# Kernel tuning notes

Measured on AMD Instinct MI355X. Metric: run time of the kernel, lower is better.

## Reference

```python
import jax, jax.numpy as jnp
import numpy as np
from jax.scipy.special import erf, digamma, i0

B, L, D, H = 4, 4096, 512, 4
_MAX_SQRT_GRADIENT = 1000.0

@jax.custom_vjp
def sqrt_bound(x):
    return jnp.sqrt(x)

def _sb_fwd(x):
    return jnp.sqrt(x), x

def _sb_bwd(x, g):
    return (g / jnp.sqrt(jnp.clip(4.0 * x, 1.0 / _MAX_SQRT_GRADIENT**2, None)),)

sqrt_bound.defvjp(_sb_fwd, _sb_bwd)

def block_diag_linear(x, w):
    # x: [..., D], w: [h, bw, bw] block-diagonal weight
    h, bw, _ = w.shape
    xr = x.reshape(x.shape[:-1] + (h, bw))
    return jnp.einsum('...hi,hij->...hj', xr, w).reshape(x.shape)

def self_att_pool(x, num_heads):
    n_state = x.shape[-1] // num_heads
    attn = jax.nn.softmax(jnp.einsum('bld,bmd->blm', x, x) / np.float32(np.sqrt(n_state)), axis=-1)
    # max over the sequence axis of the attended values, keepdims -> [B,1,D]
    return jnp.max(jnp.einsum('blm,bmd->bld', attn, x), axis=-2, keepdims=True)

def ripple_transform_hybrid(t, mix_params):
    mix = jax.nn.softmax(mix_params)
    return mix[0] * digamma(t + 1.0) + mix[1] * i0(t)

def ripple_act(data, alpha, beta, mix_params, temperature=1.0):
    def f(d):
        norm = erf(d / (jnp.max(d) * alpha))
        return jnp.sum(ripple_transform_hybrid(norm * beta, mix_params))
    g = jnp.clip(jax.grad(f)(data), -1.0, 1.0)
    return jax.nn.softmax(-g / temperature, axis=-1)  # softmin

def ripplemoe_act(data, weights, alphas, beta, mix_params, temperature=1.0):
    def f(d):
        dmax = jnp.max(d)
        norm = erf(d[None] / (dmax * alphas[:, None, None]))  # [S,B,L]
        t = ripple_transform_hybrid(norm * beta, mix_params)
        w = jax.nn.softmax(weights)
        return jnp.sum(w[:, None, None] * t)
    g = jnp.clip(jax.grad(f)(data), -1.0, 1.0)
    return jax.nn.softmax(-g / temperature, axis=-1)  # softmin

def token_selection(x, cls_w, cls_b, token_weights, prelu_a, ts_weights, ts_alphas, ts_beta, ts_mix):
    scores = jnp.einsum('bld,sd->sbl', x, cls_w) + cls_b[:, None, None]  # [S,B,L]
    p = jnp.where(scores >= 0, scores, prelu_a * scores)  # PReLU
    ts = jax.nn.celu(p) * jax.nn.silu(p) + jax.nn.gelu(p, approximate=False)
    combined = jnp.einsum('s,sbl->bl', jax.nn.selu(token_weights[:, 0]), ts)
    _, idx = jax.lax.top_k(combined, combined.shape[-1])  # k = L, descending permutation
    vals = ts.sum(0)  # [B,L]
    b_idx = jnp.arange(combined.shape[0])[:, None]
    importance = jnp.ones_like(combined).at[b_idx, idx].add(vals)
    return (1.0 + ripplemoe_act(importance, ts_weights, ts_alphas, ts_beta, ts_mix))[..., None]

def _forward(x, attention_space, W_spatial, W_sil, W_ohead, W_out, w_ig, w_ag, a_param,
             cls_w, cls_b, token_weights, prelu_a, ts_weights, ts_alphas, ts_beta, ts_mix,
             pa1_alpha, pa1_beta, pa1_mix, pa2_alpha, pa2_beta, pa2_mix):
    spatial = jnp.einsum('bld,de->ble', x, attention_space) @ W_spatial.T
    # RG-LRU style gating
    gate_x = jax.nn.sigmoid(block_diag_linear(x, w_ig))
    gate_a = jax.nn.sigmoid(block_diag_linear(x, w_ag))
    log_a = -8.0 * jax.nn.softplus(a_param) * gate_a
    normalized_x = x * gate_x * sqrt_bound(1.0 - jnp.exp(2.0 * log_a))
    gated = jnp.exp(log_a) * self_att_pool(spatial, H) + normalized_x
    sparsity = ripple_act(gated @ W_sil.T, pa1_alpha, pa1_beta, pa1_mix)
    attn = (gated * sparsity) @ W_ohead.T
    sel = token_selection(x, cls_w, cls_b, token_weights, prelu_a, ts_weights, ts_alphas, ts_beta, ts_mix)
    out = ripple_act(attn * sel, pa2_alpha, pa2_beta, pa2_mix)
    return out @ W_out.T

def setup_inputs() -> dict:
    key = jax.random.key(0)
    ks = jax.random.split(key, 12)
    lim = float(1.0 / np.sqrt(D))
    xav = float(np.sqrt(6.0 / (2 * D)))
    bw = D // H
    u = jax.random.uniform(ks[8], (D,), jnp.float32, 0.9**2 + 1e-8, 0.999**2 + 1e-8)
    return {
        'x': jax.random.normal(ks[0], (B, L, D), jnp.float32),
        'attention_space': jax.random.uniform(ks[1], (D, D), jnp.float32, -xav, xav),
        'W_spatial': jax.random.uniform(ks[2], (D, D), jnp.float32, -lim, lim),
        'W_sil': jax.random.uniform(ks[3], (D, D), jnp.float32, -lim, lim),
        'W_ohead': jax.random.uniform(ks[4], (D, D), jnp.float32, -lim, lim),
        'W_out': jax.random.uniform(ks[5], (D, D), jnp.float32, -lim, lim),
        'w_ig': jax.random.normal(ks[6], (H, bw, bw), jnp.float32) * np.float32(np.sqrt(1.0 / bw)),
        'w_ag': jax.random.normal(ks[7], (H, bw, bw), jnp.float32) * np.float32(np.sqrt(1.0 / bw)),
        'a_param': jnp.log(jnp.exp(-0.5 * jnp.log(u)) - 1.0),
        'cls_w': jax.random.uniform(ks[9], (H, D), jnp.float32, -lim, lim),
        'cls_b': jax.random.uniform(ks[10], (H,), jnp.float32, -lim, lim),
        'token_weights': jax.random.normal(ks[11], (H, 1), jnp.float32),
        'prelu_a': jnp.array(0.25, jnp.float32),
        'ts_weights': jnp.ones(H, jnp.float32) / H,
        'ts_alphas': jnp.ones(H, jnp.float32),
        'ts_beta': jnp.array(1.0, jnp.float32),
        'ts_mix': jnp.full((2,), 0.5, jnp.float32),
        'pa1_alpha': jnp.array(1.0, jnp.float32),
        'pa1_beta': jnp.array(1.0, jnp.float32),
        'pa1_mix': jnp.full((2,), 0.5, jnp.float32),
        'pa2_alpha': jnp.array(1.0, jnp.float32),
        'pa2_beta': jnp.array(1.0, jnp.float32),
        'pa2_mix': jnp.full((2,), 0.5, jnp.float32),
    }

def reference(x, attention_space, W_spatial, W_sil, W_ohead, W_out, w_ig, w_ag, a_param,
              cls_w, cls_b, token_weights, prelu_a, ts_weights, ts_alphas, ts_beta, ts_mix,
              pa1_alpha, pa1_beta, pa1_mix, pa2_alpha, pa2_beta, pa2_mix):
    return _forward(x, attention_space, W_spatial, W_sil, W_ohead, W_out, w_ig, w_ag, a_param,
                    cls_w, cls_b, token_weights, prelu_a, ts_weights, ts_alphas, ts_beta, ts_mix,
                    pa1_alpha, pa1_beta, pa1_mix, pa2_alpha, pa2_beta, pa2_mix)
```

## Files before the change

kernel.cpp:

```cpp
#include <hip/hip_runtime.h>

typedef unsigned short ushort;
typedef unsigned int uint;
typedef unsigned long long u64;

#define DEV __device__ __forceinline__

typedef __attribute__((ext_vector_type(4))) float f32x4;
typedef __bf16 bf16x8 __attribute__((ext_vector_type(8)));
typedef __attribute__((ext_vector_type(4))) ushort u16x4;
typedef __attribute__((ext_vector_type(8))) ushort u16x8;

static constexpr int B_ = 4, L_ = 4096, D_ = 512;
static constexpr long NE = (long)B_ * L_ * D_;

DEV float b2f(ushort u) { return __uint_as_float(((uint)u) << 16); }
DEV ushort f2b(float f) {
    uint u = __float_as_uint(f);
    uint r = u + 0x7FFFu + ((u >> 16) & 1u);
    return (ushort)(r >> 16);
}
DEV uint mapF(float f) {
    uint b = __float_as_uint(f);
    return (b & 0x80000000u) ? ~b : (b | 0x80000000u);
}
DEV float unmapF(uint u) {
    uint b = (u & 0x80000000u) ? (u & 0x7FFFFFFFu) : ~u;
    return __uint_as_float(b);
}
DEV float rcp_(float x) { return __builtin_amdgcn_rcpf(x); }
DEV float fexp(float x) { return __builtin_amdgcn_exp2f(x * 1.44269504089f); }
DEV float sigm(float x) { return rcp_(1.f + fexp(-x)); }

DEV void gload16(const ushort* g, ushort* l) {
    __builtin_amdgcn_global_load_lds((const __attribute__((address_space(1))) void*)g,
                                     (__attribute__((address_space(3))) void*)l, 16, 0, 0);
}

DEV int xcd_swz(int b, int nwg) {
    int q = nwg >> 3, r = nwg & 7;
    int x = b & 7, i = b >> 3;
    int base = (x < r) ? x * (q + 1) : r * (q + 1) + (x - r) * q;
    return base + i;
}

DEV float trigamma1p(float t) {
    float x = t + 1.f;
    float acc = 0.f;
#pragma unroll
    for (int k = 0; k < 6; k++) { float xx = x + (float)k; acc += rcp_(xx * xx); }
    float y = x + 6.f;
    float iy = rcp_(y), iy2 = iy * iy;
    return acc + iy * (1.f + iy * (0.5f + iy * (0.166666667f + iy2 * (-0.0333333333f + iy2 * 0.0238095238f))));
}
DEV float besselI1(float t) {
    float q = 0.25f * t * t;
    return 0.5f * t * (1.f + q * (0.5f + q * (0.0833333333f + q * (0.00694444444f + q * (3.47222222e-4f + q * 1.15740741e-5f)))));
}
DEV float rippleH(float u, float beta, float mix0, float mix1) {
    float t = beta * erff(u);
    float Tp = mix0 * trigamma1p(t) + mix1 * besselI1(t);
    float ep = 1.12837917f * fexp(-u * u);
    return beta * Tp * ep;
}

DEV void gemm_core(const ushort* __restrict__ A, int lda,
                   const ushort* __restrict__ Bt, int ldb, int K,
                   ushort* __restrict__ Alds, ushort* __restrict__ Blds,
                   f32x4 (&acc)[4][4])
{
    const int tid = threadIdx.x;
    const int lane = tid & 63;
    const int wave = tid >> 6;
    const int wr = wave >> 1, wc = wave & 1;

    const int srow = wave * 16 + (lane >> 2);
    const int skc = (lane & 3) * 8;
    const ushort* Ag0 = A + (size_t)srow * lda + skc;
    const ushort* Ag1 = A + (size_t)(srow + 64) * lda + skc;
    const ushort* Bg0 = Bt + (size_t)srow * ldb + skc;
    const ushort* Bg1 = Bt + (size_t)(srow + 64) * ldb + skc;
    const int wb = wave * 512;

    const int ar = wr * 64 + (lane & 15);
    const int br = wc * 64 + (lane & 15);
    const int kk = (lane >> 4) * 8;

    gload16(Ag0, Alds + wb);
    gload16(Ag1, Alds + 2048 + wb);
    gload16(Bg0, Blds + wb);
    gload16(Bg1, Blds + 2048 + wb);
    __syncthreads();

    int cur = 0;
    for (int k0 = 0; k0 < K; k0 += 32) {
        const int nb = cur ^ 1;
        if (k0 + 32 < K) {
            gload16(Ag0 + k0 + 32, Alds + nb * 4096 + wb);
            gload16(Ag1 + k0 + 32, Alds + nb * 4096 + 2048 + wb);
            gload16(Bg0 + k0 + 32, Blds + nb * 4096 + wb);
            gload16(Bg1 + k0 + 32, Blds + nb * 4096 + 2048 + wb);
        }
        bf16x8 af[4], bfr[4];
#pragma unroll
        for (int mi = 0; mi < 4; mi++) af[mi] = *(const bf16x8*)&Alds[cur * 4096 + (ar + mi * 16) * 32 + kk];
#pragma unroll
        for (int ni = 0; ni < 4; ni++) bfr[ni] = *(const bf16x8*)&Blds[cur * 4096 + (br + ni * 16) * 32 + kk];
#pragma unroll
        for (int mi = 0; mi < 4; mi++)
#pragma unroll
            for (int ni = 0; ni < 4; ni++)
                acc[mi][ni] = __builtin_amdgcn_mfma_f32_16x16x32_bf16(af[mi], bfr[ni], acc[mi][ni], 0, 0, 0);
        __syncthreads();
        cur = nb;
    }
}

template <int MODE, bool DOMAX>
__global__ __launch_bounds__(256, 4) void gemm_bt(
    const ushort* __restrict__ A, int lda,
    const ushort* __restrict__ Bt, int ldb,
    void* __restrict__ Cv, int ldc, int K,
    const float* __restrict__ rowScale, u64* __restrict__ pmax)
{
    __shared__ ushort Alds[2 * 128 * 32];
    __shared__ ushort Blds[2 * 128 * 32];
    const int nwg = gridDim.x * gridDim.y;
    const int s = xcd_swz(blockIdx.y * gridDim.x + blockIdx.x, nwg);
    const int bx = s % gridDim.x, by = s / gridDim.x;
    const int row0 = by * 128, col0 = bx * 128;
    f32x4 acc[4][4] = {};
    gemm_core(A + (size_t)row0 * lda, lda, Bt + (size_t)col0 * ldb, ldb, K, Alds, Blds, acc);

    const int tid = threadIdx.x;
    const int lane = tid & 63;
    const int wave = tid >> 6;
    const int wr = wave >> 1, wc = wave & 1;
    const int ocol = col0 + wc * 64 + (lane & 15);
    u64 lp = 0;
#pragma unroll
    for (int mi = 0; mi < 4; mi++) {
        const int rbase = row0 + wr * 64 + mi * 16 + (lane >> 4) * 4;
#pragma unroll
        for (int j = 0; j < 4; j++) {
            float sc = (MODE == 3) ? rowScale[rbase + j] : 1.f;
#pragma unroll
            for (int ni = 0; ni < 4; ni++) {
                float v = acc[mi][ni][j] * sc;
                int cc = ocol + ni * 16;
                if (MODE == 1) ((ushort*)Cv)[(size_t)(rbase + j) * ldc + cc] = f2b(v);
                else ((float*)Cv)[(size_t)(rbase + j) * ldc + cc] = v;
                if (DOMAX) {
                    uint idx = (uint)((rbase + j) * ldc + cc);
                    u64 p = ((u64)mapF(v) << 32) | (u64)(~idx);
                    lp = (p > lp) ? p : lp;
                }
            }
        }
    }
    if (DOMAX) {
#pragma unroll
        for (int off = 32; off > 0; off >>= 1) {
            u64 o = __shfl_xor(lp, off);
            lp = (o > lp) ? o : lp;
        }
        if (lane == 0) atomicMax(pmax, lp);
    }
}

__global__ __launch_bounds__(512, 1) void gemm256_sym_k(
    const ushort* __restrict__ spP,
    ushort* __restrict__ Sout)
{
    __shared__ ushort Alds[2 * 256 * 32];
    __shared__ ushort Blds[2 * 256 * 32];
    const int z = blockIdx.z;
    int t = xcd_swz(blockIdx.x, 136);
    int by = 0;
    while (t >= 16 - by) { t -= 16 - by; by++; }
    const int bx = by + t;
    const int row0 = by * 256, col0 = bx * 256;
    const ushort* A = spP + (size_t)z * (4096 * 512) + (size_t)row0 * 512;
    const ushort* Bt = spP + (size_t)z * (4096 * 512) + (size_t)col0 * 512;

    const int tid = threadIdx.x;
    const int lane = tid & 63;
    const int wave = tid >> 6;
    const int wr = wave >> 2, wc = wave & 3;

    const int srow = wave * 32 + (lane >> 2);
    const int skc = (lane & 3) * 8;
    const ushort* Ag0 = A + (size_t)srow * 512 + skc;
    const ushort* Ag1 = A + (size_t)(srow + 16) * 512 + skc;
    const ushort* Bg0 = Bt + (size_t)srow * 512 + skc;
    const ushort* Bg1 = Bt + (size_t)(srow + 16) * 512 + skc;
    const int wb = wave * 1024;

    const int ar = wr * 128 + (lane & 15);
    const int br = wc * 64 + (lane & 15);
    const int kk = (lane >> 4) * 8;

    f32x4 acc[8][4] = {};

    gload16(Ag0, Alds + wb);
    gload16(Ag1, Alds + wb + 512);
    gload16(Bg0, Blds + wb);
    gload16(Bg1, Blds + wb + 512);
    __syncthreads();

    int cur = 0;
    for (int k0 = 0; k0 < 512; k0 += 32) {
        const int nb = cur ^ 1;
        if (k0 + 32 < 512) {
            gload16(Ag0 + k0 + 32, Alds + nb * 8192 + wb);
            gload16(Ag1 + k0 + 32, Alds + nb * 8192 + wb + 512);
            gload16(Bg0 + k0 + 32, Blds + nb * 8192 + wb);
            gload16(Bg1 + k0 + 32, Blds + nb * 8192 + wb + 512);
        }
        bf16x8 af[8], bfr[4];
#pragma unroll
        for (int mi = 0; mi < 8; mi++) af[mi] = *(const bf16x8*)&Alds[cur * 8192 + (ar + mi * 16) * 32 + kk];
#pragma unroll
        for (int ni = 0; ni < 4; ni++) bfr[ni] = *(const bf16x8*)&Blds[cur * 8192 + (br + ni * 16) * 32 + kk];
#pragma unroll
        for (int mi = 0; mi < 8; mi++)
#pragma unroll
            for (int ni = 0; ni < 4; ni++)
                acc[mi][ni] = __builtin_amdgcn_mfma_f32_16x16x32_bf16(af[mi], bfr[ni], acc[mi][ni], 0, 0, 0);
        __syncthreads();
        cur = nb;
    }

    ushort* C = Sout + (size_t)z * 16777216;
    const int ocol = col0 + wc * 64 + (lane & 15);
#pragma unroll
    for (int mi = 0; mi < 8; mi++) {
        const int rbase = row0 + wr * 128 + mi * 16 + (lane >> 4) * 4;
#pragma unroll
        for (int j = 0; j < 4; j++)
#pragma unroll
            for (int ni = 0; ni < 4; ni++)
                C[(size_t)(rbase + j) * 4096 + ocol + ni * 16] = f2b(acc[mi][ni][j]);
    }
    if (by != bx) {
#pragma unroll
        for (int ni = 0; ni < 4; ni++) {
            const int c = ocol + ni * 16;
#pragma unroll
            for (int mi = 0; mi < 8; mi++) {
                const int r0 = row0 + wr * 128 + mi * 16 + (lane >> 4) * 4;
                u16x4 v;
#pragma unroll
                for (int j = 0; j < 4; j++) v[j] = f2b(acc[mi][ni][j]);
                *(u16x4*)&C[(size_t)c * 4096 + r0] = v;
            }
        }
    }
}

__global__ __launch_bounds__(256, 4) void pv_split_k(const ushort* __restrict__ P, const ushort* __restrict__ Vt,
                                                     float* __restrict__ part)
{
    __shared__ ushort Alds[2 * 128 * 32];
    __shared__ ushort Blds[2 * 128 * 32];
    const int ks = blockIdx.z;
    const int nwg = gridDim.x * gridDim.y;
    const int s = xcd_swz(blockIdx.y * gridDim.x + blockIdx.x, nwg);
    const int bx = s % gridDim.x, by = s / gridDim.x;
    const int row0 = by * 128, col0 = bx * 128;
    f32x4 acc[4][4] = {};
    gemm_core(P + (size_t)row0 * 4096 + ks * 1024, 4096,
              Vt + (size_t)col0 * 4096 + ks * 1024, 4096, 1024, Alds, Blds, acc);

    float* C = part + (size_t)ks * 2097152 + (size_t)row0 * 512 + col0;
    const int tid = threadIdx.x;
    const int lane = tid & 63;
    const int wave = tid >> 6;
    const int wr = wave >> 1, wc = wave & 1;
    const int ocol = wc * 64 + (lane & 15);
#pragma unroll
    for (int mi = 0; mi < 4; mi++) {
        const int rl = wr * 64 + mi * 16 + (lane >> 4) * 4;
#pragma unroll
        for (int j = 0; j < 4; j++)
#pragma unroll
            for (int ni = 0; ni < 4; ni++)
                C[(size_t)(rl + j) * 512 + ocol + ni * 16] = acc[mi][ni][j];
    }
}

__global__ __launch_bounds__(256) void pool_combine_k(const float* __restrict__ part, uint* __restrict__ poolU)
{
    const int tid = threadIdx.x;
    const int l0 = blockIdx.x * 32;
    float m0 = -3.4e38f, m1 = -3.4e38f;
    for (int l = 0; l < 32; l++) {
        size_t off = (size_t)(l0 + l) * 512;
        float s0 = 0.f, s1 = 0.f;
#pragma unroll
        for (int ks = 0; ks < 4; ks++) {
            s0 += part[(size_t)ks * 2097152 + off + tid];
            s1 += part[(size_t)ks * 2097152 + off + tid + 256];
        }
        m0 = fmaxf(m0, s0); m1 = fmaxf(m1, s1);
    }
    atomicMax(&poolU[tid], mapF(m0));
    atomicMax(&poolU[tid + 256], mapF(m1));
}

__global__ __launch_bounds__(256, 4) void gate_gemm_k(const ushort* __restrict__ xb,
                                                      const ushort* __restrict__ wigT, const ushort* __restrict__ wagT,
                                                      ushort* __restrict__ gxab, ushort* __restrict__ gaab)
{
    __shared__ ushort Alds[2 * 128 * 32];
    __shared__ ushort Blds[2 * 128 * 32];
    const int which = blockIdx.x;
    const int h = blockIdx.z;
    const ushort* A = xb + (size_t)blockIdx.y * 128 * 512 + h * 128;
    const ushort* W = (which ? wagT : wigT) + (size_t)h * 16384;
    f32x4 acc[4][4] = {};
    gemm_core(A, 512, W, 128, 128, Alds, Blds, acc);

    ushort* C = (which ? gaab : gxab) + (size_t)blockIdx.y * 128 * 512 + h * 128;
    const int tid = threadIdx.x;
    const int lane = tid & 63;
    const int wave = tid >> 6;
    const int wr = wave >> 1, wc = wave & 1;
    const int ocol = wc * 64 + (lane & 15);
#pragma unroll
    for (int mi = 0; mi < 4; mi++) {
        const int rl = wr * 64 + mi * 16 + (lane >> 4) * 4;
#pragma unroll
        for (int j = 0; j < 4; j++)
#pragma unroll
            for (int ni = 0; ni < 4; ni++)
                C[(size_t)(rl + j) * 512 + ocol + ni * 16] = f2b(acc[mi][ni][j]);
    }
}

__global__ void convert_f2b_k(const float* __restrict__ s, ushort* __restrict__ d, long n4) {
    long i = (long)blockIdx.x * blockDim.x + threadIdx.x;
    long st = (long)gridDim.x * blockDim.x;
    for (; i < n4; i += st) {
        f32x4 v = ((const f32x4*)s)[i];
        u16x4 o;
        o[0] = f2b(v[0]); o[1] = f2b(v[1]); o[2] = f2b(v[2]); o[3] = f2b(v[3]);
        ((u16x4*)d)[i] = o;
    }
}

__global__ void convert_w4_k(const float* __restrict__ w0, const float* __restrict__ w1,
                             const float* __restrict__ w2, const float* __restrict__ w3,
                             ushort* __restrict__ dst) {
    const float* srcs[4] = {w0, w1, w2, w3};
    const float* s = srcs[blockIdx.y];
    ushort* d = dst + (size_t)blockIdx.y * 262144;
    int i = blockIdx.x * 256 + threadIdx.x;
    f32x4 v = ((const f32x4*)s)[i];
    u16x4 o;
    o[0] = f2b(v[0]); o[1] = f2b(v[1]); o[2] = f2b(v[2]); o[3] = f2b(v[3]);
    ((u16x4*)d)[i] = o;
}

template <bool SRCF32>
__global__ __launch_bounds__(256) void transpose_to_bf16(const void* __restrict__ srcv, ushort* __restrict__ dst, int R, int C) {
    __shared__ float tile[32][33];
    const int z = blockIdx.z;
    const float* sf = (const float*)srcv + (size_t)z * R * C;
    const ushort* sb = (const ushort*)srcv + (size_t)z * R * C;
    ushort* dz = dst + (size_t)z * R * C;
    const int tx = threadIdx.x & 31, ty = threadIdx.x >> 5;
    const int c = blockIdx.x * 32 + tx;
#pragma unroll
    for (int k = 0; k < 4; k++) {
        const int r = blockIdx.y * 32 + ty + k * 8;
        tile[ty + k * 8][tx] = SRCF32 ? sf[(size_t)r * C + c] : b2f(sb[(size_t)r * C + c]);
    }
    __syncthreads();
#pragma unroll
    for (int k = 0; k < 4; k++) {
        const int dr = blockIdx.x * 32 + ty + k * 8;
        const int dc = blockIdx.y * 32 + tx;
        dz[(size_t)dr * R + dc] = f2b(tile[tx][ty + k * 8]);
    }
}

__global__ __launch_bounds__(256) void transpose_gates_k(const float* __restrict__ wig, const float* __restrict__ wag,
                                                         ushort* __restrict__ wigT, ushort* __restrict__ wagT) {
    __shared__ float tile[32][33];
    const int which = blockIdx.z >> 2, h = blockIdx.z & 3;
    const float* src = (which ? wag : wig) + (size_t)h * 16384;
    ushort* dst = (which ? wagT : wigT) + (size_t)h * 16384;
    const int tx = threadIdx.x & 31, ty = threadIdx.x >> 5;
    const int c = blockIdx.x * 32 + tx;
#pragma unroll
    for (int k = 0; k < 4; k++) {
        const int r = blockIdx.y * 32 + ty + k * 8;
        tile[ty + k * 8][tx] = src[(size_t)r * 128 + c];
    }
    __syncthreads();
#pragma unroll
    for (int k = 0; k < 4; k++) {
        const int dr = blockIdx.x * 32 + ty + k * 8;
        const int dc = blockIdx.y * 32 + tx;
        dst[(size_t)dr * 128 + dc] = f2b(tile[tx][ty + k * 8]);
    }
}

__global__ void init_misc_k(uint* poolU, u64* pmax) {
    int i = blockIdx.x * 256 + threadIdx.x;
    if (i < 2048) poolU[i] = 0u;
    if (i < 4) pmax[i] = 0ull;
}
__global__ void sentinel_k(float* o) { o[threadIdx.x] = 1.0e6f; }

__global__ __launch_bounds__(256) void gates_gated_k(const float* __restrict__ x, const ushort* __restrict__ gxab,
                                                     const ushort* __restrict__ gaab, const float* __restrict__ a_param,
                                                     const uint* __restrict__ poolU, ushort* __restrict__ gatedb) {
    __shared__ float sp8[512];
    const int tid = threadIdx.x;
    for (int d = tid; d < 512; d += 256) {
        float a = a_param[d];
        sp8[d] = 8.f * (fmaxf(a, 0.f) + log1pf(expf(-fabsf(a))));
    }
    __syncthreads();
    long i = (long)blockIdx.x * blockDim.x + tid;
    long st = (long)gridDim.x * blockDim.x;
    const long n8 = NE >> 3;
    for (; i < n8; i += st) {
        u16x8 gx8 = ((const u16x8*)gxab)[i];
        u16x8 ga8 = ((const u16x8*)gaab)[i];
        f32x4 x0 = ((const f32x4*)x)[2 * i];
        f32x4 x1 = ((const f32x4*)x)[2 * i + 1];
        long e = i << 3;
        int b = (int)(e >> 21);
        int d0 = (int)(e & 511);
        u16x8 o;
#pragma unroll
        for (int j = 0; j < 8; j++) {
            float xv = (j < 4) ? x0[j] : x1[j - 4];
            float gx = sigm(b2f(gx8[j]));
            float ga = sigm(b2f(ga8[j]));
            float la = -sp8[d0 + j] * ga;
            float ea = fexp(la);
            float nx = xv * gx * sqrtf(fmaxf(1.f - fexp(2.f * la), 0.f));
            float pl = unmapF(poolU[b * 512 + d0 + j]);
            o[j] = f2b(ea * pl + nx);
        }
        ((u16x8*)gatedb)[i] = o;
    }
}

__global__ __launch_bounds__(256) void softmax_rows_k(ushort* __restrict__ Sbase, float scale) {
    __shared__ float red[256];
    const int tid = threadIdx.x;
    const int r = blockIdx.x;
    ushort* row = Sbase + (size_t)(r >> 12) * 16777216 + (size_t)(r & 4095) * 4096;
    float vals[16];
    bf16x8 v0 = *(const bf16x8*)&row[tid * 16];
    bf16x8 v1 = *(const bf16x8*)&row[tid * 16 + 8];
    float mx = -3.4e38f;
#pragma unroll
    for (int k = 0; k < 8; k++) { vals[k] = (float)v0[k] * scale; mx = fmaxf(mx, vals[k]); }
#pragma unroll
    for (int k = 0; k < 8; k++) { vals[8 + k] = (float)v1[k] * scale; mx = fmaxf(mx, vals[8 + k]); }
    red[tid] = mx; __syncthreads();
    for (int s = 128; s > 0; s >>= 1) { if (tid < s) red[tid] = fmaxf(red[tid], red[tid + s]); __syncthreads(); }
    mx = red[0]; __syncthreads();
    float sum = 0.f;
#pragma unroll
    for (int k = 0; k < 16; k++) { vals[k] = fexp(vals[k] - mx); sum += vals[k]; }
    red[tid] = sum; __syncthreads();
    for (int s = 128; s > 0; s >>= 1) { if (tid < s) red[tid] += red[tid + s]; __syncthreads(); }
    float inv = rcp_(red[0]);
    u16x8 o0, o1;
#pragma unroll
    for (int k = 0; k < 8; k++) { o0[k] = f2b(vals[k] * inv); o1[k] = f2b(vals[8 + k] * inv); }
    *(u16x8*)&row[tid * 16] = o0;
    *(u16x8*)&row[tid * 16 + 8] = o1;
}

__global__ __launch_bounds__(256) void redmax1_k(const float* __restrict__ d, long n, float* __restrict__ bmax, int* __restrict__ bidx) {
    __shared__ float rv[256];
    __shared__ int ri[256];
    const int tid = threadIdx.x;
    long g = (long)blockIdx.x * 256 + tid;
    const long stride = (long)gridDim.x * 256;
    float bv = -3.4e38f; int bi = -1;
    for (long i = g; i < n; i += stride) {
        float v = d[i];
        if (v > bv) { bv = v; bi = (int)i; }
    }
    rv[tid] = bv; ri[tid] = bi; __syncthreads();
    for (int s = 128; s > 0; s >>= 1) {
        if (tid < s) {
            float ov = rv[tid + s]; int oi = ri[tid + s];
            if (oi >= 0 && (ri[tid] < 0 || ov > rv[tid] || (ov == rv[tid] && oi < ri[tid]))) { rv[tid] = ov; ri[tid] = oi; }
        }
        __syncthreads();
    }
    if (tid == 0) { bmax[blockIdx.x] = rv[0]; bidx[blockIdx.x] = ri[0]; }
}
__global__ __launch_bounds__(256) void redmax2_k(const float* __restrict__ bmax, const int* __restrict__ bidx, int n,
                                                 float* __restrict__ outM, int* __restrict__ outI) {
    __shared__ float rv[256];
    __shared__ int ri[256];
    const int tid = threadIdx.x;
    float bv = -3.4e38f; int bi = -1;
    for (int i = tid; i < n; i += 256) {
        float v = bmax[i]; int ix = bidx[i];
        if (ix >= 0 && (bi < 0 || v > bv || (v == bv && ix < bi))) { bv = v; bi = ix; }
    }
    rv[tid] = bv; ri[tid] = bi; __syncthreads();
    for (int s = 128; s > 0; s >>= 1) {
        if (tid < s) {
            float ov = rv[tid + s]; int oi = ri[tid + s];
            if (oi >= 0 && (ri[tid] < 0 || ov > rv[tid] || (ov == rv[tid] && oi < ri[tid]))) { rv[tid] = ov; ri[tid] = oi; }
        }
        __syncthreads();
    }
    if (tid == 0) { outM[0] = rv[0]; outI[0] = ri[0]; }
}

__global__ __launch_bounds__(256) void ripple_g_k(const float* __restrict__ d, float* __restrict__ gb, float* __restrict__ sspart,
                                                  const u64* __restrict__ pmax, const float* __restrict__ alpha_p,
                                                  const float* __restrict__ beta_p, const float* __restrict__ mix_p) {
    __shared__ float red[256];
    const int tid = threadIdx.x;
    const float M = unmapF((uint)(pmax[0] >> 32));
    const float alpha = alpha_p[0], beta = beta_p[0];
    float m0 = mix_p[0], m1 = mix_p[1];
    float mm = fmaxf(m0, m1);
    float e0 = fexp(m0 - mm), e1 = fexp(m1 - mm);
    float inv = rcp_(e0 + e1);
    float mix0 = e0 * inv, mix1 = e1 * inv;
    const float invMA = rcp_(M * alpha);
    float ss = 0.f;
    long g = (long)blockIdx.x * 256 + tid;
    const long stride = (long)gridDim.x * 256;
    for (long i = g; i < NE; i += stride) {
        float dv = d[i];
        float H = rippleH(dv * invMA, beta, mix0, mix1);
        gb[i] = H * invMA;
        ss += H * dv;
    }
    red[tid] = ss; __syncthreads();
    for (int s = 128; s > 0; s >>= 1) { if (tid < s) red[tid] += red[tid + s]; __syncthreads(); }
    if (tid == 0) sspart[blockIdx.x] = red[0];
}
__global__ __launch_bounds__(256) void redsum2_k(const float* __restrict__ part, int n, float* __restrict__ out) {
    __shared__ float red[256];
    const int tid = threadIdx.x;
    float s = 0.f;
    for (int i = tid; i < n; i += 256) s += part[i];
    red[tid] = s; __syncthreads();
    for (int q = 128; q > 0; q >>= 1) { if (tid < q) red[tid] += red[tid + q]; __syncthreads(); }
    if (tid == 0) out[0] = red[0];
}

template <int GS>
__global__ __launch_bounds__(256) void ripple_softmax_k(const float* __restrict__ gb,
                                                        const u64* __restrict__ pmax,
                                                        const float* __restrict__ ssTot, const float* __restrict__ alpha_p,
                                                        const ushort* __restrict__ gatedb, ushort* __restrict__ outb) {
    __shared__ float red[256];
    const int tid = threadIdx.x;
    const float M = unmapF((uint)(pmax[0] >> 32));
    const int amax = (int)(~(uint)(pmax[0] & 0xFFFFFFFFull));
    const float corr = ssTot[0] * rcp_(M * M * alpha_p[0]);
    long base = (long)blockIdx.x * 512;
    float g0 = gb[base + tid];
    float g1 = gb[base + tid + 256];
    if ((int)(base + tid) == amax) g0 -= corr;
    if ((int)(base + tid + 256) == amax) g1 -= corr;
    g0 = fminf(fmaxf(g0, -1.f), 1.f);
    g1 = fminf(fmaxf(g1, -1.f), 1.f);
    float mn = fminf(g0, g1);
    red[tid] = mn; __syncthreads();
    for (int s = 128; s > 0; s >>= 1) { if (tid < s) red[tid] = fminf(red[tid], red[tid + s]); __syncthreads(); }
    mn = red[0]; __syncthreads();
    float e0 = fexp(mn - g0), e1 = fexp(mn - g1);
    red[tid] = e0 + e1; __syncthreads();
    for (int s = 128; s > 0; s >>= 1) { if (tid < s) red[tid] += red[tid + s]; __syncthreads(); }
    float inv = rcp_(red[0]);
    if (GS) {
        outb[base + tid] = f2b(b2f(gatedb[base + tid]) * (e0 * inv));
        outb[base + tid + 256] = f2b(b2f(gatedb[base + tid + 256]) * (e1 * inv));
    } else {
        outb[base + tid] = f2b(e0 * inv);
        outb[base + tid + 256] = f2b(e1 * inv);
    }
}

__global__ __launch_bounds__(256) void ts1_k(const float* __restrict__ x, const float* __restrict__ cls_w,
                                             const float* __restrict__ cls_b, const float* __restrict__ tw,
                                             const float* __restrict__ prelu_a,
                                             float* __restrict__ combined, float* __restrict__ vals) {
    __shared__ float cw[2048];
    const int tid = threadIdx.x;
    for (int i = tid; i < 2048; i += 256) cw[i] = cls_w[i];
    __syncthreads();
    const int lane = tid & 63, wid = tid >> 6;
    const int row = blockIdx.x * 4 + wid;
    const float* xr = x + (size_t)row * 512 + lane * 8;
    float pa0 = 0, pa1 = 0, pa2 = 0, pa3 = 0;
#pragma unroll
    for (int j = 0; j < 8; j++) {
        float v = xr[j];
        int c = lane * 8 + j;
        pa0 += v * cw[c]; pa1 += v * cw[512 + c]; pa2 += v * cw[1024 + c]; pa3 += v * cw[1536 + c];
    }
#pragma unroll
    for (int o = 32; o > 0; o >>= 1) {
        pa0 += __shfl_down(pa0, o); pa1 += __shfl_down(pa1, o);
        pa2 += __shfl_down(pa2, o); pa3 += __shfl_down(pa3, o);
    }
    if (lane == 0) {
        float a = prelu_a[0];
        float sc[4] = {pa0, pa1, pa2, pa3};
        float comb = 0.f, vsum = 0.f;
#pragma unroll
        for (int s = 0; s < 4; s++) {
            float p = sc[s] + cls_b[s];
            p = (p >= 0.f) ? p : a * p;
            float cel = (p > 0.f) ? p : expm1f(p);
            float sil = p * sigm(p);
            float gel = 0.5f * p * (1.f + erff(p * 0.70710678f));
            float ts = cel * sil + gel;
            float ww = tw[s];
            float se = 1.05070099f * ((ww > 0.f) ? ww : 1.67326324f * expm1f(ww));
            comb += se * ts;
            vsum += ts;
        }
        combined[row] = comb;
        vals[row] = vsum;
    }
}

__global__ __launch_bounds__(256) void ts2a_k(const float* __restrict__ combined, int* __restrict__ rankp) {
    __shared__ float q[512];
    const int b = blockIdx.z;
    const int tid = threadIdx.x;
    const float* cr = combined + b * 4096;
    const int q0 = blockIdx.y * 512;
    for (int i = tid; i < 512; i += 256) q[i] = cr[q0 + i];
    __syncthreads();
    const int p = blockIdx.x * 256 + tid;
    const float cp = cr[p];
    const f32x4* q4 = (const f32x4*)q;
    int rank = 0;
#pragma unroll 8
    for (int i4 = 0; i4 < 128; i4++) {
        f32x4 v = q4[i4];
        int qb = q0 + i4 * 4;
        rank += (v[0] > cp) || (v[0] == cp && (qb + 0) < p);
        rank += (v[1] > cp) || (v[1] == cp && (qb + 1) < p);
        rank += (v[2] > cp) || (v[2] == cp && (qb + 2) < p);
        rank += (v[3] > cp) || (v[3] == cp && (qb + 3) < p);
    }
    rankp[((b * 8 + blockIdx.y) * 4096) + p] = rank;
}

__global__ __launch_bounds__(256) void ts2b_k(const int* __restrict__ rankp, const float* __restrict__ vals,
                                              float* __restrict__ imp) {
    const int b = blockIdx.y;
    const int p = blockIdx.x * 256 + threadIdx.x;
    int rank = 0;
#pragma unroll
    for (int c = 0; c < 8; c++) rank += rankp[((b * 8 + c) * 4096) + p];
    imp[b * 4096 + p] = 1.f + vals[b * 4096 + rank];
}

__global__ __launch_bounds__(256) void moe_g_k(const float* __restrict__ imp, float* __restrict__ gmoe,
                                               float* __restrict__ sspart, const float* __restrict__ scalM,
                                               const float* __restrict__ tsw, const float* __restrict__ tsa,
                                               const float* __restrict__ tsb, const float* __restrict__ tsmix) {
    __shared__ float red[256];
    const int tid = threadIdx.x;
    const float M = scalM[0];
    float w[4], invMA[4], invA[4];
    {
        float wm = fmaxf(fmaxf(tsw[0], tsw[1]), fmaxf(tsw[2], tsw[3]));
        float s = 0.f;
#pragma unroll
        for (int k = 0; k < 4; k++) { w[k] = fexp(tsw[k] - wm); s += w[k]; }
        float si = rcp_(s);
#pragma unroll
        for (int k = 0; k < 4; k++) { w[k] *= si; invMA[k] = rcp_(M * tsa[k]); invA[k] = rcp_(tsa[k]); }
    }
    const float beta = tsb[0];
    float m0 = tsmix[0], m1 = tsmix[1];
    float mm = fmaxf(m0, m1);
    float e0 = fexp(m0 - mm), e1 = fexp(m1 - mm);
    float minv = rcp_(e0 + e1);
    const float mix0 = e0 * minv, mix1 = e1 * minv;

    float ss = 0.f;
    int i = blockIdx.x * 256 + tid;
    const int stride = gridDim.x * 256;
    for (; i < 65536; i += stride) {
        float dv = imp[i];
        float gbv = 0.f;
#pragma unroll
        for (int s = 0; s < 4; s++) {
            float H = rippleH(dv * invMA[s], beta, mix0, mix1);
            gbv += w[s] * H * invMA[s];
            ss += w[s] * H * dv * invA[s];
        }
        gmoe[i] = gbv;
    }
    red[tid] = ss; __syncthreads();
    for (int s = 128; s > 0; s >>= 1) { if (tid < s) red[tid] += red[tid + s]; __syncthreads(); }
    if (tid == 0) sspart[blockIdx.x] = red[0];
}

__global__ __launch_bounds__(256) void moe_sel_k(const float* __restrict__ gmoe, const float* __restrict__ scalM,
                                                 const int* __restrict__ scalI, const float* __restrict__ ssTot,
                                                 float* __restrict__ sel) {
    __shared__ float red[256];
    const int tid = threadIdx.x;
    const int b = blockIdx.x;
    const float M = scalM[0];
    const int amax = scalI[0];
    const float corr = ssTot[0] * rcp_(M * M);
    float g[16];
    float mn = 3.4e38f;
#pragma unroll
    for (int k = 0; k < 16; k++) {
        int i = b * 4096 + tid + k * 256;
        float v = gmoe[i];
        if (i == amax) v -= corr;
        v = fminf(fmaxf(v, -1.f), 1.f);
        g[k] = v;
        mn = fminf(mn, v);
    }
    red[tid] = mn; __syncthreads();
    for (int s = 128; s > 0; s >>= 1) { if (tid < s) red[tid] = fminf(red[tid], red[tid + s]); __syncthreads(); }
    mn = red[0]; __syncthreads();
    float sum = 0.f;
#pragma unroll
    for (int k = 0; k < 16; k++) { g[k] = fexp(mn - g[k]); sum += g[k]; }
    red[tid] = sum; __syncthreads();
    for (int s = 128; s > 0; s >>= 1) { if (tid < s) red[tid] += red[tid + s]; __syncthreads(); }
    float inv = rcp_(red[0]);
#pragma unroll
    for (int k = 0; k < 16; k++) sel[b * 4096 + tid + k * 256] = 1.f + g[k] * inv;
}

static constexpr size_t OFF_XB    = 0;
static constexpr size_t OFF_TMPB  = 16777216;
static constexpr size_t OFF_SPB   = 33554432;
static constexpr size_t OFF_SPT   = 50331648;
static constexpr size_t OFF_DBUF  = 67108864;
static constexpr size_t OFF_HBUF  = 100663296;
static constexpr size_t OFF_GATB  = 134217728;
static constexpr size_t OFF_NXB   = 150994944;
static constexpr size_t OFF_EAB   = 167772160;
static constexpr size_t OFF_AST   = 184549376;
static constexpr size_t OFF_WSP   = 185073664;
static constexpr size_t OFF_WSIL  = 185597952;
static constexpr size_t OFF_WOH   = 186122240;
static constexpr size_t OFF_WOUT  = 186646528;
static constexpr size_t OFF_WIGT  = 187170816;
static constexpr size_t OFF_WAGT  = 187301888;
static constexpr size_t OFF_POOL  = 187432960;
static constexpr size_t OFF_SCAL  = 187441152;
static constexpr size_t OFF_SCALI = 187441408;
static constexpr size_t OFF_BMAX  = 187441664;
static constexpr size_t OFF_BIDX  = 187449856;
static constexpr size_t OFF_SSP   = 187458048;
static constexpr size_t OFF_COMB  = 187466240;
static constexpr size_t OFF_VALS  = 187728384;
static constexpr size_t OFF_IMP   = 187990528;
static constexpr size_t OFF_GMOE  = 188252672;
static constexpr size_t OFF_SEL   = 188514816;
static constexpr size_t WS_NEED   = 188776960;

extern "C" void kernel_launch(void* const* d_in, const int* in_sizes, int n_in,
                              void* d_out, int out_size, void* d_ws, size_t ws_size,
                              hipStream_t stream)
{
    (void)in_sizes; (void)n_in; (void)out_size;
    const float* x    = (const float*)d_in[0];
    const float* AS   = (const float*)d_in[1];
    const float* Wsp  = (const float*)d_in[2];
    const float* Wsil = (const float*)d_in[3];
    const float* Woh  = (const float*)d_in[4];
    const float* Wout = (const float*)d_in[5];
    const float* wig  = (const float*)d_in[6];
    const float* wag  = (const float*)d_in[7];
    const float* a_param = (const float*)d_in[8];
    const float* cls_w = (const float*)d_in[9];
    const float* cls_b = (const float*)d_in[10];
    const float* tokw  = (const float*)d_in[11];
    const float* prelu = (const float*)d_in[12];
    const float* tsw   = (const float*)d_in[13];
    const float* tsa   = (const float*)d_in[14];
    const float* tsb   = (const float*)d_in[15];
    const float* tsmix = (const float*)d_in[16];
    const float* p1a = (const float*)d_in[17];
    const float* p1b = (const float*)d_in[18];
    const float* p1m = (const float*)d_in[19];
    const float* p2a = (const float*)d_in[20];
    const float* p2b = (const float*)d_in[21];
    const float* p2m = (const float*)d_in[22];
    float* out = (float*)d_out;

    char* w = (char*)d_ws;
    if (ws_size < WS_NEED) { sentinel_k<<<1, 256, 0, stream>>>(out); return; }

    ushort* xb    = (ushort*)(w + OFF_XB);
    ushort* tmpb  = (ushort*)(w + OFF_TMPB);
    ushort* spb   = (ushort*)(w + OFF_SPB);
    ushort* spT   = (ushort*)(w + OFF_SPT);
    float*  dbuf  = (float*)(w + OFF_DBUF);
    float*  Hbuf  = (float*)(w + OFF_HBUF);
    ushort* Spair = (ushort*)(w + OFF_DBUF);
    float*  pvpart= (float*)(w + OFF_XB);
    int*    rankp = (int*)(w + OFF_DBUF);
    ushort* gatedb= (ushort*)(w + OFF_GATB);
    ushort* gxab  = (ushort*)(w + OFF_NXB);
    ushort* gaab  = (ushort*)(w + OFF_EAB);
    ushort* ASt   = (ushort*)(w + OFF_AST);
    ushort* Wspb  = (ushort*)(w + OFF_WSP);
    ushort* Wsilb = (ushort*)(w + OFF_WSIL);
    ushort* Wohb  = (ushort*)(w + OFF_WOH);
    ushort* Woutb = (ushort*)(w + OFF_WOUT);
    ushort* wigT  = (ushort*)(w + OFF_WIGT);
    ushort* wagT  = (ushort*)(w + OFF_WAGT);
    uint*   poolU = (uint*)(w + OFF_POOL);
    float*  scal  = (float*)(w + OFF_SCAL);
    u64*    pmax  = (u64*)(w + OFF_SCAL + 128);
    int*    scalI = (int*)(w + OFF_SCALI);
    float*  bmax  = (float*)(w + OFF_BMAX);
    int*    bidx  = (int*)(w + OFF_BIDX);
    float*  sspart= (float*)(w + OFF_SSP);
    float*  comb  = (float*)(w + OFF_COMB);
    float*  vals  = (float*)(w + OFF_VALS);
    float*  imp   = (float*)(w + OFF_IMP);
    float*  gmoe  = (float*)(w + OFF_GMOE);
    float*  sel   = (float*)(w + OFF_SEL);
    ushort* gsb     = tmpb;
    ushort* probs2b = xb;

    convert_f2b_k<<<2048, 256, 0, stream>>>(x, xb, NE >> 2);
    convert_w4_k<<<dim3(256, 4), 256, 0, stream>>>(Wsp, Wsil, Woh, Wout, Wspb);
    transpose_to_bf16<true><<<dim3(16, 16, 1), 256, 0, stream>>>(AS, ASt, 512, 512);
    transpose_gates_k<<<dim3(4, 4, 8), 256, 0, stream>>>(wig, wag, wigT, wagT);
    init_misc_k<<<8, 256, 0, stream>>>(poolU, pmax);

    gate_gemm_k<<<dim3(2, 128, 4), 256, 0, stream>>>(xb, wigT, wagT, gxab, gaab);

    gemm_bt<1, false><<<dim3(4, 128), 256, 0, stream>>>(xb, 512, ASt, 512, tmpb, 512, 512, nullptr, nullptr);
    gemm_bt<1, false><<<dim3(4, 128), 256, 0, stream>>>(tmpb, 512, Wspb, 512, spb, 512, 512, nullptr, nullptr);

    transpose_to_bf16<false><<<dim3(16, 128, 4), 256, 0, stream>>>(spb, spT, 4096, 512);
    const float sc128 = 0.0883883476f;
    for (int p = 0; p < 2; p++) {
        const ushort* spP = spb + (size_t)(2 * p) * L_ * D_;
        gemm256_sym_k<<<dim3(136, 1, 2), 512, 0, stream>>>(spP, Spair);
        softmax_rows_k<<<8192, 256, 0, stream>>>(Spair, sc128);
        for (int z = 0; z < 2; z++) {
            const int b = 2 * p + z;
            pv_split_k<<<dim3(4, 32, 4), 256, 0, stream>>>(Spair + (size_t)z * 16777216,
                                                           spT + (size_t)b * D_ * L_, pvpart);
            pool_combine_k<<<128, 256, 0, stream>>>(pvpart, poolU + b * 512);
        }
    }

    gates_gated_k<<<1024, 256, 0, stream>>>(x, gxab, gaab, a_param, poolU, gatedb);

    gemm_bt<0, true><<<dim3(4, 128), 256, 0, stream>>>(gatedb, 512, Wsilb, 512, dbuf, 512, 512, nullptr, &pmax[0]);
    ripple_g_k<<<2048, 256, 0, stream>>>(dbuf, Hbuf, sspart, &pmax[0], p1a, p1b, p1m);
    redsum2_k<<<1, 256, 0, stream>>>(sspart, 2048, &scal[1]);
    ripple_softmax_k<1><<<16384, 256, 0, stream>>>(Hbuf, &pmax[0], &scal[1], p1a, gatedb, gsb);

    ts1_k<<<4096, 256, 0, stream>>>(x, cls_w, cls_b, tokw, prelu, comb, vals);
    ts2a_k<<<dim3(16, 8, 4), 256, 0, stream>>>(comb, rankp);
    ts2b_k<<<dim3(16, 4), 256, 0, stream>>>(rankp, vals, imp);
    redmax1_k<<<64, 256, 0, stream>>>(imp, 65536, bmax, bidx);
    redmax2_k<<<1, 256, 0, stream>>>(bmax, bidx, 64, &scal[4], &scalI[2]);
    moe_g_k<<<64, 256, 0, stream>>>(imp, gmoe, sspart, &scal[4], tsw, tsa, tsb, tsmix);
    redsum2_k<<<1, 256, 0, stream>>>(sspart, 64, &scal[5]);
    moe_sel_k<<<4, 256, 0, stream>>>(gmoe, &scal[4], &scalI[2], &scal[5], sel);

    gemm_bt<3, true><<<dim3(4, 128), 256, 0, stream>>>(gsb, 512, Wohb, 512, dbuf, 512, 512, sel, &pmax[1]);

    ripple_g_k<<<2048, 256, 0, stream>>>(dbuf, Hbuf, sspart, &pmax[1], p2a, p2b, p2m);
    redsum2_k<<<1, 256, 0, stream>>>(sspart, 2048, &scal[3]);
    ripple_softmax_k<0><<<16384, 256, 0, stream>>>(Hbuf, &pmax[1], &scal[3], p2a, nullptr, probs2b);

    gemm_bt<0, false><<<dim3(4, 128), 256, 0, stream>>>(probs2b, 512, Woutb, 512, out, 512, 512, nullptr, nullptr);
}
```

Baseline: 657.4 us.

## Fuse exp and row sums into score GEMM, defer softmax normalization to pooling

The score GEMM now applies exp(scale*s) directly in its epilogue and atomically accumulates row sums, dropping the separate softmax_rows pass over the 4096x4096 matrices. Normalization moves into pool_combine by scaling each row's PV result by the reciprocal row sum. The GEMM runs over the full grid instead of the symmetric upper triangle, so it does about twice the MFMA work in exchange for removing a full read and write of the score matrix. Dropping max subtraction risks overflow when scores are large. Two small reductions are also folded into neighbouring kernels (redmax1 into ts2b, redsum2 into moe_sel) to cut launches.

```diff
diff --git a/kernel.cpp b/kernel.cpp
--- a/kernel.cpp
+++ b/kernel.cpp
@@ -168,17 +168,17 @@
     }
 }
 
-__global__ __launch_bounds__(512, 1) void gemm256_sym_k(
+__global__ __launch_bounds__(512, 4) void gemm256_exp_k(
     const ushort* __restrict__ spP,
-    ushort* __restrict__ Sout)
+    ushort* __restrict__ Sout,
+    float* __restrict__ rowsum)
 {
     __shared__ ushort Alds[2 * 256 * 32];
     __shared__ ushort Blds[2 * 256 * 32];
     const int z = blockIdx.z;
-    int t = xcd_swz(blockIdx.x, 136);
-    int by = 0;
-    while (t >= 16 - by) { t -= 16 - by; by++; }
-    const int bx = by + t;
+    const int nwg = gridDim.x * gridDim.y;
+    const int s = xcd_swz(blockIdx.y * gridDim.x + blockIdx.x, nwg);
+    const int bx = s % gridDim.x, by = s / gridDim.x;
     const int row0 = by * 256, col0 = bx * 256;
     const ushort* A = spP + (size_t)z * (4096 * 512) + (size_t)row0 * 512;
     const ushort* Bt = spP + (size_t)z * (4096 * 512) + (size_t)col0 * 512;
@@ -232,28 +232,24 @@
     }
 
     ushort* C = Sout + (size_t)z * 16777216;
+    float* rs = rowsum + z * 4096;
+    const float sc128 = 0.0883883476f;
     const int ocol = col0 + wc * 64 + (lane & 15);
 #pragma unroll
     for (int mi = 0; mi < 8; mi++) {
         const int rbase = row0 + wr * 128 + mi * 16 + (lane >> 4) * 4;
 #pragma unroll
-        for (int j = 0; j < 4; j++)
-#pragma unroll
-            for (int ni = 0; ni < 4; ni++)
-                C[(size_t)(rbase + j) * 4096 + ocol + ni * 16] = f2b(acc[mi][ni][j]);
-    }
-    if (by != bx) {
-#pragma unroll
-        for (int ni = 0; ni < 4; ni++) {
-            const int c = ocol + ni * 16;
-#pragma unroll
-            for (int mi = 0; mi < 8; mi++) {
-                const int r0 = row0 + wr * 128 + mi * 16 + (lane >> 4) * 4;
-                u16x4 v;
-#pragma unroll
-                for (int j = 0; j < 4; j++) v[j] = f2b(acc[mi][ni][j]);
-                *(u16x4*)&C[(size_t)c * 4096 + r0] = v;
+        for (int j = 0; j < 4; j++) {
+            float rsum = 0.f;
+#pragma unroll
+            for (int ni = 0; ni < 4; ni++) {
+                float p = fexp(acc[mi][ni][j] * sc128);
+                C[(size_t)(rbase + j) * 4096 + ocol + ni * 16] = f2b(p);
+                rsum += p;
             }
+#pragma unroll
+            for (int off = 1; off < 16; off <<= 1) rsum += __shfl_xor(rsum, off);
+            if ((lane & 15) == 0) atomicAdd(&rs[rbase + j], rsum);
         }
     }
 }
@@ -289,20 +285,22 @@
     }
 }
 
-__global__ __launch_bounds__(256) void pool_combine_k(const float* __restrict__ part, uint* __restrict__ poolU)
+__global__ __launch_bounds__(256) void pool_combine_k(const float* __restrict__ part, const float* __restrict__ rs,
+                                                      uint* __restrict__ poolU)
 {
     const int tid = threadIdx.x;
     const int l0 = blockIdx.x * 32;
     float m0 = -3.4e38f, m1 = -3.4e38f;
     for (int l = 0; l < 32; l++) {
         size_t off = (size_t)(l0 + l) * 512;
+        float iv = rcp_(rs[l0 + l]);
         float s0 = 0.f, s1 = 0.f;
 #pragma unroll
         for (int ks = 0; ks < 4; ks++) {
             s0 += part[(size_t)ks * 2097152 + off + tid];
             s1 += part[(size_t)ks * 2097152 + off + tid + 256];
         }
-        m0 = fmaxf(m0, s0); m1 = fmaxf(m1, s1);
+        m0 = fmaxf(m0, s0 * iv); m1 = fmaxf(m1, s1 * iv);
     }
     atomicMax(&poolU[tid], mapF(m0));
     atomicMax(&poolU[tid + 256], mapF(m1));
@@ -411,6 +409,9 @@
     int i = blockIdx.x * 256 + threadIdx.x;
     if (i < 2048) poolU[i] = 0u;
     if (i < 4) pmax[i] = 0ull;
+}
+__global__ void zero_rs_k(float* rs) {
+    rs[blockIdx.x * 256 + threadIdx.x] = 0.f;
 }
 __global__ void sentinel_k(float* o) { o[threadIdx.x] = 1.0e6f; }
 
@@ -451,56 +452,6 @@
     }
 }
 
-__global__ __launch_bounds__(256) void softmax_rows_k(ushort* __restrict__ Sbase, float scale) {
-    __shared__ float red[256];
-    const int tid = threadIdx.x;
-    const int r = blockIdx.x;
-    ushort* row = Sbase + (size_t)(r >> 12) * 16777216 + (size_t)(r & 4095) * 4096;
-    float vals[16];
-    bf16x8 v0 = *(const bf16x8*)&row[tid * 16];
-    bf16x8 v1 = *(const bf16x8*)&row[tid * 16 + 8];
-    float mx = -3.4e38f;
-#pragma unroll
-    for (int k = 0; k < 8; k++) { vals[k] = (float)v0[k] * scale; mx = fmaxf(mx, vals[k]); }
-#pragma unroll
-    for (int k = 0; k < 8; k++) { vals[8 + k] = (float)v1[k] * scale; mx = fmaxf(mx, vals[8 + k]); }
-    red[tid] = mx; __syncthreads();
-    for (int s = 128; s > 0; s >>= 1) { if (tid < s) red[tid] = fmaxf(red[tid], red[tid + s]); __syncthreads(); }
-    mx = red[0]; __syncthreads();
-    float sum = 0.f;
-#pragma unroll
-    for (int k = 0; k < 16; k++) { vals[k] = fexp(vals[k] - mx); sum += vals[k]; }
-    red[tid] = sum; __syncthreads();
-    for (int s = 128; s > 0; s >>= 1) { if (tid < s) red[tid] += red[tid + s]; __syncthreads(); }
-    float inv = rcp_(red[0]);
-    u16x8 o0, o1;
-#pragma unroll
-    for (int k = 0; k < 8; k++) { o0[k] = f2b(vals[k] * inv); o1[k] = f2b(vals[8 + k] * inv); }
-    *(u16x8*)&row[tid * 16] = o0;
-    *(u16x8*)&row[tid * 16 + 8] = o1;
-}
-
-__global__ __launch_bounds__(256) void redmax1_k(const float* __restrict__ d, long n, float* __restrict__ bmax, int* __restrict__ bidx) {
-    __shared__ float rv[256];
-    __shared__ int ri[256];
-    const int tid = threadIdx.x;
-    long g = (long)blockIdx.x * 256 + tid;
-    const long stride = (long)gridDim.x * 256;
-    float bv = -3.4e38f; int bi = -1;
-    for (long i = g; i < n; i += stride) {
-        float v = d[i];
-        if (v > bv) { bv = v; bi = (int)i; }
-    }
-    rv[tid] = bv; ri[tid] = bi; __syncthreads();
-    for (int s = 128; s > 0; s >>= 1) {
-        if (tid < s) {
-            float ov = rv[tid + s]; int oi = ri[tid + s];
-            if (oi >= 0 && (ri[tid] < 0 || ov > rv[tid] || (ov == rv[tid] && oi < ri[tid]))) { rv[tid] = ov; ri[tid] = oi; }
-        }
-        __syncthreads();
-    }
-    if (tid == 0) { bmax[blockIdx.x] = rv[0]; bidx[blockIdx.x] = ri[0]; }
-}
 __global__ __launch_bounds__(256) void redmax2_k(const float* __restrict__ bmax, const int* __restrict__ bidx, int n,
                                                  float* __restrict__ outM, int* __restrict__ outI) {
     __shared__ float rv[256];
@@ -662,13 +613,27 @@
 }
 
 __global__ __launch_bounds__(256) void ts2b_k(const int* __restrict__ rankp, const float* __restrict__ vals,
-                                              float* __restrict__ imp) {
+                                              float* __restrict__ imp, float* __restrict__ bmax, int* __restrict__ bidx) {
+    __shared__ float rv[256];
+    __shared__ int ri[256];
+    const int tid = threadIdx.x;
     const int b = blockIdx.y;
-    const int p = blockIdx.x * 256 + threadIdx.x;
+    const int p = blockIdx.x * 256 + tid;
     int rank = 0;
 #pragma unroll
     for (int c = 0; c < 8; c++) rank += rankp[((b * 8 + c) * 4096) + p];
-    imp[b * 4096 + p] = 1.f + vals[b * 4096 + rank];
+    const int gi = b * 4096 + p;
+    const float v = 1.f + vals[b * 4096 + rank];
+    imp[gi] = v;
+    rv[tid] = v; ri[tid] = gi; __syncthreads();
+    for (int s = 128; s > 0; s >>= 1) {
+        if (tid < s) {
+            float ov = rv[tid + s]; int oi = ri[tid + s];
+            if (ov > rv[tid] || (ov == rv[tid] && oi < ri[tid])) { rv[tid] = ov; ri[tid] = oi; }
+        }
+        __syncthreads();
+    }
+    if (tid == 0) { bmax[b * 16 + blockIdx.x] = rv[0]; bidx[b * 16 + blockIdx.x] = ri[0]; }
 }
 
 __global__ __launch_bounds__(256) void moe_g_k(const float* __restrict__ imp, float* __restrict__ gmoe,
@@ -715,14 +680,17 @@
 }
 
 __global__ __launch_bounds__(256) void moe_sel_k(const float* __restrict__ gmoe, const float* __restrict__ scalM,
-                                                 const int* __restrict__ scalI, const float* __restrict__ ssTot,
+                                                 const int* __restrict__ scalI, const float* __restrict__ sspart,
                                                  float* __restrict__ sel) {
     __shared__ float red[256];
     const int tid = threadIdx.x;
     const int b = blockIdx.x;
     const float M = scalM[0];
     const int amax = scalI[0];
-    const float corr = ssTot[0] * rcp_(M * M);
+    float ssTot = 0.f;
+#pragma unroll
+    for (int k = 0; k < 64; k++) ssTot += sspart[k];
+    const float corr = ssTot * rcp_(M * M);
     float g[16];
     float mn = 3.4e38f;
 #pragma unroll
@@ -836,6 +804,7 @@
     int*    bidx  = (int*)(w + OFF_BIDX);
     float*  sspart= (float*)(w + OFF_SSP);
     float*  comb  = (float*)(w + OFF_COMB);
+    float*  rowsum= comb;
     float*  vals  = (float*)(w + OFF_VALS);
     float*  imp   = (float*)(w + OFF_IMP);
     float*  gmoe  = (float*)(w + OFF_GMOE);
@@ -855,16 +824,15 @@
     gemm_bt<1, false><<<dim3(4, 128), 256, 0, stream>>>(tmpb, 512, Wspb, 512, spb, 512, 512, nullptr, nullptr);
 
     transpose_to_bf16<false><<<dim3(16, 128, 4), 256, 0, stream>>>(spb, spT, 4096, 512);
-    const float sc128 = 0.0883883476f;
     for (int p = 0; p < 2; p++) {
         const ushort* spP = spb + (size_t)(2 * p) * L_ * D_;
-        gemm256_sym_k<<<dim3(136, 1, 2), 512, 0, stream>>>(spP, Spair);
-        softmax_rows_k<<<8192, 256, 0, stream>>>(Spair, sc128);
+        zero_rs_k<<<32, 256, 0, stream>>>(rowsum);
+        gemm256_exp_k<<<dim3(16, 16, 2), 512, 0, stream>>>(spP, Spair, rowsum);
         for (int z = 0; z < 2; z++) {
             const int b = 2 * p + z;
             pv_split_k<<<dim3(4, 32, 4), 256, 0, stream>>>(Spair + (size_t)z * 16777216,
                                                            spT + (size_t)b * D_ * L_, pvpart);
-            pool_combine_k<<<128, 256, 0, stream>>>(pvpart, poolU + b * 512);
+            pool_combine_k<<<128, 256, 0, stream>>>(pvpart, rowsum + z * 4096, poolU + b * 512);
         }
     }
 
@@ -877,12 +845,10 @@
 
     ts1_k<<<4096, 256, 0, stream>>>(x, cls_w, cls_b, tokw, prelu, comb, vals);
     ts2a_k<<<dim3(16, 8, 4), 256, 0, stream>>>(comb, rankp);
-    ts2b_k<<<dim3(16, 4), 256, 0, stream>>>(rankp, vals, imp);
-    redmax1_k<<<64, 256, 0, stream>>>(imp, 65536, bmax, bidx);
+    ts2b_k<<<dim3(16, 4), 256, 0, stream>>>(rankp, vals, imp, bmax, bidx);
     redmax2_k<<<1, 256, 0, stream>>>(bmax, bidx, 64, &scal[4], &scalI[2]);
     moe_g_k<<<64, 256, 0, stream>>>(imp, gmoe, sspart, &scal[4], tsw, tsa, tsb, tsmix);
-    redsum2_k<<<1, 256, 0, stream>>>(sspart, 64, &scal[5]);
-    moe_sel_k<<<4, 256, 0, stream>>>(gmoe, &scal[4], &scalI[2], &scal[5], sel);
+    moe_sel_k<<<4, 256, 0, stream>>>(gmoe, &scal[4], &scalI[2], sspart, sel);
 
     gemm_bt<3, true><<<dim3(4, 128), 256, 0, stream>>>(gsb, 512, Wohb, 512, dbuf, 512, 512, sel, &pmax[1]);
 
```

After: 1.124 ms. 1.71x slower.
